# Performance work log

Hardware: AMD Instinct MI355X
Metric: run time of the kernel (lower is better)

Reference implementation:

```python
import jax, jax.numpy as jnp
import numpy as np

N, D, K = 8192, 4096, 8
F_HID = D // 4  # 1024


def setup_inputs() -> dict:
    key = jax.random.key(0)
    ks = jax.random.split(key, 8)
    s1 = 1.0 / np.sqrt(2 * D)
    s2 = 1.0 / np.sqrt(F_HID)
    sr = 1.0 / np.sqrt(D)
    return {
        "h_anchor": jax.random.normal(ks[0], (N, D), jnp.float32),
        "h_mask": jax.random.normal(ks[1], (N, D), jnp.float32),
        "Wr": jax.random.normal(ks[2], (K, D), jnp.float32) * sr,
        "br": jnp.zeros((K,), jnp.float32),
        "W1": jax.random.normal(ks[3], (K, F_HID, 2 * D), jnp.float32) * s1,
        "b1": jnp.zeros((K, F_HID), jnp.float32),
        "W2": jax.random.normal(ks[4], (K, D, F_HID), jnp.float32) * s2,
        "b2": jnp.zeros((K, D), jnp.float32),
    }


def reference(h_anchor, h_mask, Wr, br, W1, b1, W2, b2):
    # routing weights: softmax(h_mask @ Wr^T + br) -> [N, K]
    weights = jax.nn.softmax(h_mask @ Wr.T + br, axis=-1)
    # conditioned input: [N, 2D]
    conditioned = jnp.concatenate([h_anchor, h_mask], axis=-1)
    # all-expert first GEMM: [K, N, F]
    h1 = jnp.einsum("nc,kfc->knf", conditioned, W1) + b1[:, None, :]
    h1 = jax.nn.gelu(h1, approximate=False)  # torch nn.GELU default = exact erf
    # second GEMM: [K, N, D]
    expert_out = jnp.einsum("knf,kdf->knd", h1, W2) + b2[:, None, :]
    # softmax-weighted combine over experts -> [N, D]
    return jnp.einsum("knd,nk->nd", expert_out, weights)
```

## Files before the change

### kernel.cpp

```cpp
#include <hip/hip_runtime.h>
#include <hip/hip_bf16.h>
#include <math.h>

typedef __bf16 bf16_t;
typedef __bf16 bf16x4 __attribute__((ext_vector_type(4)));
typedef __bf16 bf16x8 __attribute__((ext_vector_type(8)));
typedef float  f32x4  __attribute__((ext_vector_type(4)));
typedef float  f32x16 __attribute__((ext_vector_type(16)));

#define AS1 __attribute__((address_space(1)))
#define AS3 __attribute__((address_space(3)))

__device__ __forceinline__ void gload_lds16(const bf16_t* g, char* l) {
  __builtin_amdgcn_global_load_lds((const AS1 void*)g, (AS3 void*)l, 16, 0, 0);
}

static constexpr int N_ROWS = 8192;
static constexpr int DDIM   = 4096;
static constexpr int KEXP   = 8;
static constexpr int FHID   = 1024;
static constexpr int KD     = 8192;
static constexpr int NKT    = KD / 64;


__global__ __launch_bounds__(256)
void routing_kernel(const float* __restrict__ hm, const float* __restrict__ Wr,
                    const float* __restrict__ br, float* __restrict__ wgt) {
  const int n = blockIdx.x;
  const int t = threadIdx.x;
  const int wid = t >> 6;
  const float4* row = (const float4*)(hm + (size_t)n * DDIM);
  float4 x[4];
#pragma unroll
  for (int j = 0; j < 4; ++j) x[j] = row[t + j * 256];
  __shared__ float red[KEXP][4];
  float part[KEXP];
#pragma unroll
  for (int k = 0; k < KEXP; ++k) {
    const float4* wr = (const float4*)(Wr + (size_t)k * DDIM);
    float s = 0.f;
#pragma unroll
    for (int j = 0; j < 4; ++j) {
      float4 w4 = wr[t + j * 256];
      s += x[j].x * w4.x + x[j].y * w4.y + x[j].z * w4.z + x[j].w * w4.w;
    }
#pragma unroll
    for (int off = 32; off > 0; off >>= 1) s += __shfl_down(s, off);
    part[k] = s;
  }
  if ((t & 63) == 0) {
#pragma unroll
    for (int k = 0; k < KEXP; ++k) red[k][wid] = part[k];
  }
  __syncthreads();
  if (t == 0) {
    float lg[KEXP];
    float mx = -1e30f;
#pragma unroll
    for (int k = 0; k < KEXP; ++k) {
      lg[k] = red[k][0] + red[k][1] + red[k][2] + red[k][3] + br[k];
      mx = fmaxf(mx, lg[k]);
    }
    float sum = 0.f;
#pragma unroll
    for (int k = 0; k < KEXP; ++k) { lg[k] = expf(lg[k] - mx); sum += lg[k]; }
    float inv = 1.f / sum;
#pragma unroll
    for (int k = 0; k < KEXP; ++k) wgt[(size_t)n * KEXP + k] = lg[k] * inv;
  }
}

__device__ __forceinline__ bf16x4 cvt4(float4 v) {
  bf16x4 o;
  o[0] = (bf16_t)v.x; o[1] = (bf16_t)v.y; o[2] = (bf16_t)v.z; o[3] = (bf16_t)v.w;
  return o;
}

__global__ __launch_bounds__(256)
void pack_cond_kernel(const float* __restrict__ ha, const float* __restrict__ hm,
                      bf16_t* __restrict__ Apk) {
  const int bm = blockIdx.x >> 7, t = blockIdx.x & 127;
  const int tid = threadIdx.x;
  const float* src = (t < 64) ? ha : hm;
  const int cb = (t & 63) * 64;
  __shared__ char pb[32768];
#pragma unroll
  for (int i = 0; i < 16; ++i) {
    int u = i * 256 + tid;
    int r = u >> 4, c = (u & 15) * 4;
    float4 v = *(const float4*)(src + (size_t)(bm * 256 + r) * DDIM + cb + c);
    int off = ((r >> 7) & 1) * 16384 + ((c >> 4) & 3) * 4096 + ((r >> 5) & 3) * 1024
            + ((c >> 3) & 1) * 512 + (r & 31) * 16 + (c & 7) * 2;
    *(bf16x4*)(pb + off) = cvt4(v);
  }
  __syncthreads();
  char* dst = (char*)Apk + (size_t)blockIdx.x * 32768;
#pragma unroll
  for (int i = 0; i < 8; ++i) {
    int off = i * 4096 + tid * 16;
    *(float4*)(dst + off) = *(const float4*)(pb + off);
  }
}

__global__ __launch_bounds__(256)
void pack_w1_kernel(const float* __restrict__ W1, bf16_t* __restrict__ Bpk) {
  const int bn = blockIdx.x >> 7, t = blockIdx.x & 127;
  const int tid = threadIdx.x;
  __shared__ char pb[32768];
#pragma unroll
  for (int i = 0; i < 16; ++i) {
    int u = i * 256 + tid;
    int r = u >> 4, c = (u & 15) * 4;
    float4 v = *(const float4*)(W1 + (size_t)(bn * 256 + r) * KD + t * 64 + c);
    int off = ((c >> 4) & 3) * 8192 + ((r >> 5) & 7) * 1024
            + ((c >> 3) & 1) * 512 + (r & 31) * 16 + (c & 7) * 2;
    *(bf16x4*)(pb + off) = cvt4(v);
  }
  __syncthreads();
  char* dst = (char*)Bpk + (size_t)blockIdx.x * 32768;
#pragma unroll
  for (int i = 0; i < 8; ++i) {
    int off = i * 4096 + tid * 16;
    *(float4*)(dst + off) = *(const float4*)(pb + off);
  }
}

__global__ __launch_bounds__(256)
void pack_w2_kernel(const float* __restrict__ W2, bf16_t* __restrict__ Bpk) {
  const int bn = blockIdx.x >> 7, t = blockIdx.x & 127;
  const int tid = threadIdx.x;
  const int ke = t >> 4, f0 = (t & 15) * 64;
  __shared__ char pb[32768];
#pragma unroll
  for (int i = 0; i < 16; ++i) {
    int u = i * 256 + tid;
    int r = u >> 4, c = (u & 15) * 4;
    float4 v = *(const float4*)(W2 + ((size_t)ke * DDIM + bn * 256 + r) * FHID + f0 + c);
    int off = ((c >> 4) & 3) * 8192 + ((r >> 5) & 7) * 1024
            + ((c >> 3) & 1) * 512 + (r & 31) * 16 + (c & 7) * 2;
    *(bf16x4*)(pb + off) = cvt4(v);
  }
  __syncthreads();
  char* dst = (char*)Bpk + (size_t)blockIdx.x * 32768;
#pragma unroll
  for (int i = 0; i < 8; ++i) {
    int off = i * 4096 + tid * 16;
    *(float4*)(dst + off) = *(const float4*)(pb + off);
  }
}

template <int MODE, int NCOLS>
__global__ __launch_bounds__(256, 1)
void gemm256_kernel(const bf16_t* __restrict__ Apk, const bf16_t* __restrict__ Bpk,
                    void* __restrict__ Cout, const float* __restrict__ bias,
                    const float* __restrict__ wgt) {
  __shared__ char lds_raw[2 * 65536];

  const int tid  = threadIdx.x;
  const int wid  = tid >> 6;
  const int lane = tid & 63;
  const int wr   = wid >> 1;
  const int wc   = wid & 1;

  constexpr int NBN    = NCOLS / 256;
  constexpr int NWIN_N = NBN / 16;
  const int bid = blockIdx.x;
  const int w   = bid >> 8;
  const int sl  = bid & 255;
  const int xcd = sl & 7;
  const int cu  = sl >> 3;
  const int wm  = w / NWIN_N, wn = w % NWIN_N;
  const int bm  = wm * 16 + ((xcd >> 1) << 2) + (cu & 3);
  const int bn  = wn * 16 + ((xcd & 1) << 3) + (cu >> 2);
  const int arow0 = bm * 256;
  const int brow0 = bn * 256;

  const size_t abase = (size_t)bm * NKT * 16384;
  const size_t bbase = (size_t)bn * NKT * 16384;
  const size_t ssub  = (size_t)(wid * 512 + lane * 8);
  const int    dsto  = wid << 10;

  const char* A0 = lds_raw + wr * 16384 + lane * 16;
  const char* B0 = lds_raw + 32768 + wc * 4096 + lane * 16;
  const char* A1 = A0 + 65536;
  const char* B1 = B0 + 65536;

  f32x16 acc[4][4];
#pragma unroll
  for (int mi = 0; mi < 4; ++mi)
#pragma unroll
    for (int nj = 0; nj < 4; ++nj)
#pragma unroll
      for (int r = 0; r < 16; ++r) acc[mi][nj][r] = 0.f;

  bf16x8 xa0, xa1, xa2, xa3, xb0, xb1, xb2, xb3;
  bf16x8 ya0, ya1, ya2, ya3, yb0, yb1, yb2, yb3;

#define SB __builtin_amdgcn_sched_barrier(0);
#define LG0 asm volatile("s_waitcnt lgkmcnt(0)" ::: "memory"); SB

#define STGA(C, TAU, NB)                                                         \
  gload_lds16(Apk + abase + (size_t)((TAU) & (NKT - 1)) * 16384 + (C) * 2048 + ssub, \
              (NB) + (C) * 4096 + dsto);
#define STGB(C, TAU, NB)                                                         \
  gload_lds16(Bpk + bbase + (size_t)((TAU) & (NKT - 1)) * 16384 + (C) * 2048 + ssub, \
              (NB) + 32768 + (C) * 4096 + dsto);

#define RDA4(P, BASE, S)                                                        \
  P##a0 = *(const bf16x8*)((BASE) + (S) * 4096);                                \
  P##a1 = *(const bf16x8*)((BASE) + (S) * 4096 + 1024);                         \
  P##a2 = *(const bf16x8*)((BASE) + (S) * 4096 + 2048);                         \
  P##a3 = *(const bf16x8*)((BASE) + (S) * 4096 + 3072);                         \
  SB
#define RDB4(P, BASE, S)                                                        \
  P##b0 = *(const bf16x8*)((BASE) + (S) * 8192);                                \
  P##b1 = *(const bf16x8*)((BASE) + (S) * 8192 + 1024);                         \
  P##b2 = *(const bf16x8*)((BASE) + (S) * 8192 + 2048);                         \
  P##b3 = *(const bf16x8*)((BASE) + (S) * 8192 + 3072);                         \
  SB

#define MF4(P, MI)                                                              \
  acc[MI][0] = __builtin_amdgcn_mfma_f32_32x32x16_bf16(P##a##MI, P##b0,         \
                                                       acc[MI][0], 0, 0, 0);    \
  acc[MI][1] = __builtin_amdgcn_mfma_f32_32x32x16_bf16(P##a##MI, P##b1,         \
                                                       acc[MI][1], 0, 0, 0);    \
  acc[MI][2] = __builtin_amdgcn_mfma_f32_32x32x16_bf16(P##a##MI, P##b2,         \
                                                       acc[MI][2], 0, 0, 0);    \
  acc[MI][3] = __builtin_amdgcn_mfma_f32_32x32x16_bf16(P##a##MI, P##b3,         \
                                                       acc[MI][3], 0, 0, 0);    \
  SB

#define TILE(T, CA, CB, NB)                                                     \
  RDA4(x, CA, 0) RDB4(x, CB, 0)                                                 \
  LG0                                                                           \
  MF4(x, 0) RDA4(y, CA, 1)                                                      \
  MF4(x, 1) RDB4(y, CB, 1)                                                      \
  MF4(x, 2) STGA(0, (T) + 1, NB) STGA(1, (T) + 1, NB)                           \
            STGA(2, (T) + 1, NB) STGA(3, (T) + 1, NB) SB                        \
  MF4(x, 3) STGA(4, (T) + 1, NB) STGA(5, (T) + 1, NB)                           \
            STGA(6, (T) + 1, NB) STGA(7, (T) + 1, NB) SB                        \
  LG0                                                                           \
  MF4(y, 0) RDA4(x, CA, 2)                                                      \
  MF4(y, 1) RDB4(x, CB, 2)                                                      \
  MF4(y, 2) STGB(0, (T) + 1, NB) STGB(1, (T) + 1, NB)                           \
            STGB(2, (T) + 1, NB) STGB(3, (T) + 1, NB) SB                        \
  MF4(y, 3) STGB(4, (T) + 1, NB) STGB(5, (T) + 1, NB)                           \
            STGB(6, (T) + 1, NB) STGB(7, (T) + 1, NB) SB                        \
  LG0                                                                           \
  MF4(x, 0) RDA4(y, CA, 3)                                                      \
  MF4(x, 1) RDB4(y, CB, 3)                                                      \
  MF4(x, 2) MF4(x, 3)                                                           \
  LG0                                                                           \
  MF4(y, 0) MF4(y, 1) MF4(y, 2) MF4(y, 3)                                       \
  asm volatile("s_waitcnt vmcnt(0)" ::: "memory");                              \
  SB                                                                            \
  __builtin_amdgcn_s_barrier();                                                 \
  SB

#pragma unroll
  for (int c = 0; c < 8; ++c) { STGA(c, 0, lds_raw) }
#pragma unroll
  for (int c = 0; c < 8; ++c) { STGB(c, 0, lds_raw) }
  asm volatile("s_waitcnt vmcnt(0)" ::: "memory");
  __builtin_amdgcn_s_barrier();
  SB

  for (int t = 0; t < NKT; t += 2) {
    TILE(t, A0, B0, lds_raw + 65536)
    TILE(t + 1, A1, B1, lds_raw)
  }
#undef TILE
#undef MF4
#undef RDA4
#undef RDB4
#undef STGA
#undef STGB
#undef LG0
#undef SB

  const int rbase = arow0 + wr * 128 + ((lane >> 5) << 2);
  const int cbase = brow0 + wc * 128 + (lane & 31);

  if constexpr (MODE == 1) {
    char* __restrict__ Hc = (char*)Cout;
    const int kexp = brow0 >> 10;
    float bv[4];
    size_t cpart[4];
#pragma unroll
    for (int nj = 0; nj < 4; ++nj) {
      int c = cbase + nj * 32;
      bv[nj] = bias[c];
      cpart[nj] = (size_t)(c >> 6) * 32768 + ((c >> 4) & 3) * 4096
                + ((c >> 3) & 1) * 512 + (c & 7) * 2;
    }
#pragma unroll
    for (int mi = 0; mi < 4; ++mi)
#pragma unroll
      for (int r = 0; r < 16; ++r) {
        int n = rbase + mi * 32 + (r & 3) + 8 * (r >> 2);
        float wn4 = wgt[(size_t)n * KEXP + kexp];
        size_t npart = (size_t)(n >> 8) * (NKT * 32768) + ((n >> 7) & 1) * 16384
                     + ((n >> 5) & 3) * 1024 + (n & 31) * 16;
#pragma unroll
        for (int nj = 0; nj < 4; ++nj) {
          float x = acc[mi][nj][r] + bv[nj];
          float g = 0.5f * x * (1.f + erff(x * 0.70710678118654752f));
          *(bf16_t*)(Hc + npart + cpart[nj]) = (bf16_t)(g * wn4);
        }
      }
  } else {
    float* __restrict__ O = (float*)Cout;
    float bc[4][KEXP];
#pragma unroll
    for (int nj = 0; nj < 4; ++nj)
#pragma unroll
      for (int k = 0; k < KEXP; ++k)
        bc[nj][k] = bias[(size_t)k * NCOLS + cbase + nj * 32];
#pragma unroll
    for (int mi = 0; mi < 4; ++mi)
#pragma unroll
      for (int r = 0; r < 16; ++r) {
        int n = rbase + mi * 32 + (r & 3) + 8 * (r >> 2);
        const float4* wp = (const float4*)(wgt + (size_t)n * KEXP);
        float4 wa = wp[0], wb = wp[1];
        float w8[KEXP] = {wa.x, wa.y, wa.z, wa.w, wb.x, wb.y, wb.z, wb.w};
#pragma unroll
        for (int nj = 0; nj < 4; ++nj) {
          float s = 0.f;
#pragma unroll
          for (int k = 0; k < KEXP; ++k) s += w8[k] * bc[nj][k];
          O[(size_t)n * NCOLS + cbase + nj * 32] = acc[mi][nj][r] + s;
        }
      }
  }
}

extern "C" void kernel_launch(void* const* d_in, const int* in_sizes, int n_in,
                              void* d_out, int out_size, void* d_ws, size_t ws_size,
                              hipStream_t stream) {
  const float* h_anchor = (const float*)d_in[0];
  const float* h_mask   = (const float*)d_in[1];
  const float* Wr       = (const float*)d_in[2];
  const float* br       = (const float*)d_in[3];
  const float* W1       = (const float*)d_in[4];
  const float* b1       = (const float*)d_in[5];
  const float* W2       = (const float*)d_in[6];
  const float* b2       = (const float*)d_in[7];
  float* out = (float*)d_out;

  char* ws = (char*)d_ws;
  bf16_t* Apk  = (bf16_t*)(ws);
  bf16_t* B1pk = (bf16_t*)(ws + ((size_t)128 << 20));
  bf16_t* B2pk = (bf16_t*)(ws + ((size_t)256 << 20));
  bf16_t* Hpk  = (bf16_t*)(ws + ((size_t)320 << 20));
  float*  wgt  = (float*) (ws + ((size_t)448 << 20));

  routing_kernel<<<N_ROWS, 256, 0, stream>>>(h_mask, Wr, br, wgt);
  pack_cond_kernel<<<32 * 128, 256, 0, stream>>>(h_anchor, h_mask, Apk);
  pack_w1_kernel<<<32 * 128, 256, 0, stream>>>(W1, B1pk);
  pack_w2_kernel<<<16 * 128, 256, 0, stream>>>(W2, B2pk);

  gemm256_kernel<1, 8192><<<(N_ROWS / 256) * (KD / 256), 256, 0, stream>>>(
      Apk, B1pk, (void*)Hpk, b1, wgt);
  gemm256_kernel<2, 4096><<<(N_ROWS / 256) * (DDIM / 256), 256, 0, stream>>>(
      Hpk, B2pk, (void*)out, b2, wgt);
}
```

Baseline: 1.789 ms.

## Restructure GEMM to 256x128 tiles with 512 threads and triple-buffered K=32 pipeline

```diff
diff --git a/kernel.cpp b/kernel.cpp
--- a/kernel.cpp
+++ b/kernel.cpp
@@ -6,7 +6,6 @@
 typedef __bf16 bf16x4 __attribute__((ext_vector_type(4)));
 typedef __bf16 bf16x8 __attribute__((ext_vector_type(8)));
 typedef float  f32x4  __attribute__((ext_vector_type(4)));
-typedef float  f32x16 __attribute__((ext_vector_type(16)));
 
 #define AS1 __attribute__((address_space(1)))
 #define AS3 __attribute__((address_space(3)))
@@ -20,7 +19,8 @@
 static constexpr int KEXP   = 8;
 static constexpr int FHID   = 1024;
 static constexpr int KD     = 8192;
-static constexpr int NKT    = KD / 64;
+static constexpr int NKT64  = KD / 64;
+static constexpr int NKT32  = KD / 32;
 
 
 __global__ __launch_bounds__(256)
@@ -150,11 +150,11 @@
 }
 
 template <int MODE, int NCOLS>
-__global__ __launch_bounds__(256, 1)
-void gemm256_kernel(const bf16_t* __restrict__ Apk, const bf16_t* __restrict__ Bpk,
-                    void* __restrict__ Cout, const float* __restrict__ bias,
-                    const float* __restrict__ wgt) {
-  __shared__ char lds_raw[2 * 65536];
+__global__ __launch_bounds__(512, 4)
+void gemm_kernel(const bf16_t* __restrict__ Apk, const bf16_t* __restrict__ Bpk,
+                 void* __restrict__ Cout, const float* __restrict__ bias,
+                 const float* __restrict__ wgt) {
+  __shared__ char lds[3 * 24576];
 
   const int tid  = threadIdx.x;
   const int wid  = tid >> 6;
@@ -162,7 +162,7 @@
   const int wr   = wid >> 1;
   const int wc   = wid & 1;
 
-  constexpr int NBN    = NCOLS / 256;
+  constexpr int NBN    = NCOLS / 128;
   constexpr int NWIN_N = NBN / 16;
   const int bid = blockIdx.x;
   const int w   = bid >> 8;
@@ -173,122 +173,116 @@
   const int bm  = wm * 16 + ((xcd >> 1) << 2) + (cu & 3);
   const int bn  = wn * 16 + ((xcd & 1) << 3) + (cu >> 2);
   const int arow0 = bm * 256;
-  const int brow0 = bn * 256;
-
-  const size_t abase = (size_t)bm * NKT * 16384;
-  const size_t bbase = (size_t)bn * NKT * 16384;
-  const size_t ssub  = (size_t)(wid * 512 + lane * 8);
-  const int    dsto  = wid << 10;
-
-  const char* A0 = lds_raw + wr * 16384 + lane * 16;
-  const char* B0 = lds_raw + 32768 + wc * 4096 + lane * 16;
-  const char* A1 = A0 + 65536;
-  const char* B1 = B0 + 65536;
-
-  f32x16 acc[4][4];
+  const int bcol0 = bn * 128;
+
+  const char* Abase = (const char*)Apk + (size_t)bm * NKT64 * 32768;
+  const char* Bbase = (const char*)Bpk + (size_t)(bn >> 1) * NKT64 * 32768;
+  const int pA0 = 2 * wid, pA1 = 2 * wid + 1, qB = wid;
+  const int a0s = (pA0 >> 3) * 16384 + ((pA0 >> 2) & 1) * 4096 + (pA0 & 3) * 1024;
+  const int a1s = (pA1 >> 3) * 16384 + ((pA1 >> 2) & 1) * 4096 + (pA1 & 3) * 1024;
+  const int a0d = (pA0 >> 3) * 8192 + ((pA0 >> 2) & 1) * 4096 + (pA0 & 3) * 1024;
+  const int a1d = (pA1 >> 3) * 8192 + ((pA1 >> 2) & 1) * 4096 + (pA1 & 3) * 1024;
+  const int bqs = (qB >> 2) * 8192 + ((bn & 1) * 4 + (qB & 3)) * 1024;
+  const int bqd = 16384 + (qB >> 2) * 4096 + (qB & 3) * 1024;
+
+  const int lpart = (lane & 15) * 16 + ((lane >> 4) & 1) * 512 + (lane >> 5) * 4096;
+  int aoff[4], boff[4];
 #pragma unroll
   for (int mi = 0; mi < 4; ++mi)
-#pragma unroll
-    for (int nj = 0; nj < 4; ++nj)
-#pragma unroll
-      for (int r = 0; r < 16; ++r) acc[mi][nj][r] = 0.f;
-
-  bf16x8 xa0, xa1, xa2, xa3, xb0, xb1, xb2, xb3;
-  bf16x8 ya0, ya1, ya2, ya3, yb0, yb1, yb2, yb3;
+    aoff[mi] = (wr >> 1) * 8192 + ((wr & 1) * 2 + (mi >> 1)) * 1024 + (mi & 1) * 256 + lpart;
+#pragma unroll
+  for (int nj = 0; nj < 4; ++nj)
+    boff[nj] = 16384 + (wc * 2 + (nj >> 1)) * 1024 + (nj & 1) * 256 + lpart;
+
+  f32x4 acc[4][4];
+  f32x4 zero = {0.f, 0.f, 0.f, 0.f};
+#pragma unroll
+  for (int mi = 0; mi < 4; ++mi)
+#pragma unroll
+    for (int nj = 0; nj < 4; ++nj) acc[mi][nj] = zero;
 
 #define SB __builtin_amdgcn_sched_barrier(0);
-#define LG0 asm volatile("s_waitcnt lgkmcnt(0)" ::: "memory"); SB
-
-#define STGA(C, TAU, NB)                                                         \
-  gload_lds16(Apk + abase + (size_t)((TAU) & (NKT - 1)) * 16384 + (C) * 2048 + ssub, \
-              (NB) + (C) * 4096 + dsto);
-#define STGB(C, TAU, NB)                                                         \
-  gload_lds16(Bpk + bbase + (size_t)((TAU) & (NKT - 1)) * 16384 + (C) * 2048 + ssub, \
-              (NB) + 32768 + (C) * 4096 + dsto);
-
-#define RDA4(P, BASE, S)                                                        \
-  P##a0 = *(const bf16x8*)((BASE) + (S) * 4096);                                \
-  P##a1 = *(const bf16x8*)((BASE) + (S) * 4096 + 1024);                         \
-  P##a2 = *(const bf16x8*)((BASE) + (S) * 4096 + 2048);                         \
-  P##a3 = *(const bf16x8*)((BASE) + (S) * 4096 + 3072);                         \
+#define STG3(KT, BUF)                                                            \
+  {                                                                              \
+    const int kt_ = (KT) & (NKT32 - 1);                                          \
+    const size_t t64 = (size_t)(kt_ >> 1) * 32768;                               \
+    const int klo = (kt_ & 1) * 2;                                               \
+    gload_lds16((const bf16_t*)(Abase + t64 + a0s + klo * 4096 + lane * 16),     \
+                (BUF) + a0d);                                                    \
+    gload_lds16((const bf16_t*)(Abase + t64 + a1s + klo * 4096 + lane * 16),     \
+                (BUF) + a1d);                                                    \
+    gload_lds16((const bf16_t*)(Bbase + t64 + bqs + klo * 8192 + lane * 16),     \
+                (BUF) + bqd);                                                    \
+  }
+
+  STG3(0, lds) STG3(1, lds + 24576) SB
+  asm volatile("s_waitcnt vmcnt(3)" ::: "memory");
   SB
-#define RDB4(P, BASE, S)                                                        \
-  P##b0 = *(const bf16x8*)((BASE) + (S) * 8192);                                \
-  P##b1 = *(const bf16x8*)((BASE) + (S) * 8192 + 1024);                         \
-  P##b2 = *(const bf16x8*)((BASE) + (S) * 8192 + 2048);                         \
-  P##b3 = *(const bf16x8*)((BASE) + (S) * 8192 + 3072);                         \
-  SB
-
-#define MF4(P, MI)                                                              \
-  acc[MI][0] = __builtin_amdgcn_mfma_f32_32x32x16_bf16(P##a##MI, P##b0,         \
-                                                       acc[MI][0], 0, 0, 0);    \
-  acc[MI][1] = __builtin_amdgcn_mfma_f32_32x32x16_bf16(P##a##MI, P##b1,         \
-                                                       acc[MI][1], 0, 0, 0);    \
-  acc[MI][2] = __builtin_amdgcn_mfma_f32_32x32x16_bf16(P##a##MI, P##b2,         \
-                                                       acc[MI][2], 0, 0, 0);    \
-  acc[MI][3] = __builtin_amdgcn_mfma_f32_32x32x16_bf16(P##a##MI, P##b3,         \
-                                                       acc[MI][3], 0, 0, 0);    \
-  SB
-
-#define TILE(T, CA, CB, NB)                                                     \
-  RDA4(x, CA, 0) RDB4(x, CB, 0)                                                 \
-  LG0                                                                           \
-  MF4(x, 0) RDA4(y, CA, 1)                                                      \
-  MF4(x, 1) RDB4(y, CB, 1)                                                      \
-  MF4(x, 2) STGA(0, (T) + 1, NB) STGA(1, (T) + 1, NB)                           \
-            STGA(2, (T) + 1, NB) STGA(3, (T) + 1, NB) SB                        \
-  MF4(x, 3) STGA(4, (T) + 1, NB) STGA(5, (T) + 1, NB)                           \
-            STGA(6, (T) + 1, NB) STGA(7, (T) + 1, NB) SB                        \
-  LG0                                                                           \
-  MF4(y, 0) RDA4(x, CA, 2)                                                      \
-  MF4(y, 1) RDB4(x, CB, 2)                                                      \
-  MF4(y, 2) STGB(0, (T) + 1, NB) STGB(1, (T) + 1, NB)                           \
-            STGB(2, (T) + 1, NB) STGB(3, (T) + 1, NB) SB                        \
-  MF4(y, 3) STGB(4, (T) + 1, NB) STGB(5, (T) + 1, NB)                           \
-            STGB(6, (T) + 1, NB) STGB(7, (T) + 1, NB) SB                        \
-  LG0                                                                           \
-  MF4(x, 0) RDA4(y, CA, 3)                                                      \
-  MF4(x, 1) RDB4(y, CB, 3)                                                      \
-  MF4(x, 2) MF4(x, 3)                                                           \
-  LG0                                                                           \
-  MF4(y, 0) MF4(y, 1) MF4(y, 2) MF4(y, 3)                                       \
-  asm volatile("s_waitcnt vmcnt(0)" ::: "memory");                              \
-  SB                                                                            \
-  __builtin_amdgcn_s_barrier();                                                 \
-  SB
-
-#pragma unroll
-  for (int c = 0; c < 8; ++c) { STGA(c, 0, lds_raw) }
-#pragma unroll
-  for (int c = 0; c < 8; ++c) { STGB(c, 0, lds_raw) }
-  asm volatile("s_waitcnt vmcnt(0)" ::: "memory");
   __builtin_amdgcn_s_barrier();
   SB
 
-  for (int t = 0; t < NKT; t += 2) {
-    TILE(t, A0, B0, lds_raw + 65536)
-    TILE(t + 1, A1, B1, lds_raw)
-  }
-#undef TILE
-#undef MF4
-#undef RDA4
-#undef RDB4
-#undef STGA
-#undef STGB
-#undef LG0
+  char* rb = lds;
+  char* mb = lds + 24576;
+  char* sb = lds + 49152;
+
+#pragma unroll 1
+  for (int t = 0; t < NKT32; ++t) {
+    STG3(t + 2, sb) SB
+    bf16x8 a0, a1, a2, a3, b0, b1, b2, b3;
+    a0 = *(const bf16x8*)(rb + aoff[0]); SB
+    a1 = *(const bf16x8*)(rb + aoff[1]); SB
+    a2 = *(const bf16x8*)(rb + aoff[2]); SB
+    a3 = *(const bf16x8*)(rb + aoff[3]); SB
+    b0 = *(const bf16x8*)(rb + boff[0]); SB
+    b1 = *(const bf16x8*)(rb + boff[1]); SB
+    b2 = *(const bf16x8*)(rb + boff[2]); SB
+    b3 = *(const bf16x8*)(rb + boff[3]); SB
+    __builtin_amdgcn_s_setprio(1);
+    asm volatile("s_waitcnt lgkmcnt(3)" ::: "memory"); SB
+    acc[0][0] = __builtin_amdgcn_mfma_f32_16x16x32_bf16(a0, b0, acc[0][0], 0, 0, 0);
+    acc[1][0] = __builtin_amdgcn_mfma_f32_16x16x32_bf16(a1, b0, acc[1][0], 0, 0, 0);
+    acc[2][0] = __builtin_amdgcn_mfma_f32_16x16x32_bf16(a2, b0, acc[2][0], 0, 0, 0);
+    acc[3][0] = __builtin_amdgcn_mfma_f32_16x16x32_bf16(a3, b0, acc[3][0], 0, 0, 0);
+    SB
+    asm volatile("s_waitcnt lgkmcnt(2)" ::: "memory"); SB
+    acc[0][1] = __builtin_amdgcn_mfma_f32_16x16x32_bf16(a0, b1, acc[0][1], 0, 0, 0);
+    acc[1][1] = __builtin_amdgcn_mfma_f32_16x16x32_bf16(a1, b1, acc[1][1], 0, 0, 0);
+    acc[2][1] = __builtin_amdgcn_mfma_f32_16x16x32_bf16(a2, b1, acc[2][1], 0, 0, 0);
+    acc[3][1] = __builtin_amdgcn_mfma_f32_16x16x32_bf16(a3, b1, acc[3][1], 0, 0, 0);
+    SB
+    asm volatile("s_waitcnt lgkmcnt(1)" ::: "memory"); SB
+    acc[0][2] = __builtin_amdgcn_mfma_f32_16x16x32_bf16(a0, b2, acc[0][2], 0, 0, 0);
+    acc[1][2] = __builtin_amdgcn_mfma_f32_16x16x32_bf16(a1, b2, acc[1][2], 0, 0, 0);
+    acc[2][2] = __builtin_amdgcn_mfma_f32_16x16x32_bf16(a2, b2, acc[2][2], 0, 0, 0);
+    acc[3][2] = __builtin_amdgcn_mfma_f32_16x16x32_bf16(a3, b2, acc[3][2], 0, 0, 0);
+    SB
+    asm volatile("s_waitcnt lgkmcnt(0)" ::: "memory"); SB
+    acc[0][3] = __builtin_amdgcn_mfma_f32_16x16x32_bf16(a0, b3, acc[0][3], 0, 0, 0);
+    acc[1][3] = __builtin_amdgcn_mfma_f32_16x16x32_bf16(a1, b3, acc[1][3], 0, 0, 0);
+    acc[2][3] = __builtin_amdgcn_mfma_f32_16x16x32_bf16(a2, b3, acc[2][3], 0, 0, 0);
+    acc[3][3] = __builtin_amdgcn_mfma_f32_16x16x32_bf16(a3, b3, acc[3][3], 0, 0, 0);
+    SB
+    __builtin_amdgcn_s_setprio(0);
+    asm volatile("s_waitcnt vmcnt(3)" ::: "memory");
+    SB
+    __builtin_amdgcn_s_barrier();
+    SB
+    char* tmp = rb; rb = mb; mb = sb; sb = tmp;
+  }
+#undef STG3
 #undef SB
 
-  const int rbase = arow0 + wr * 128 + ((lane >> 5) << 2);
-  const int cbase = brow0 + wc * 128 + (lane & 31);
+  const int rbase = arow0 + wr * 64 + ((lane >> 4) << 2);
+  const int cbase = bcol0 + wc * 64 + (lane & 15);
 
   if constexpr (MODE == 1) {
     char* __restrict__ Hc = (char*)Cout;
-    const int kexp = brow0 >> 10;
+    const int kexp = bcol0 >> 10;
     float bv[4];
     size_t cpart[4];
 #pragma unroll
     for (int nj = 0; nj < 4; ++nj) {
-      int c = cbase + nj * 32;
+      int c = cbase + nj * 16;
       bv[nj] = bias[c];
       cpart[nj] = (size_t)(c >> 6) * 32768 + ((c >> 4) & 3) * 4096
                 + ((c >> 3) & 1) * 512 + (c & 7) * 2;
@@ -296,10 +290,10 @@
 #pragma unroll
     for (int mi = 0; mi < 4; ++mi)
 #pragma unroll
-      for (int r = 0; r < 16; ++r) {
-        int n = rbase + mi * 32 + (r & 3) + 8 * (r >> 2);
+      for (int r = 0; r < 4; ++r) {
+        int n = rbase + mi * 16 + r;
         float wn4 = wgt[(size_t)n * KEXP + kexp];
-        size_t npart = (size_t)(n >> 8) * (NKT * 32768) + ((n >> 7) & 1) * 16384
+        size_t npart = (size_t)(n >> 8) * (NKT64 * 32768) + ((n >> 7) & 1) * 16384
                      + ((n >> 5) & 3) * 1024 + (n & 31) * 16;
 #pragma unroll
         for (int nj = 0; nj < 4; ++nj) {
@@ -315,12 +309,12 @@
     for (int nj = 0; nj < 4; ++nj)
 #pragma unroll
       for (int k = 0; k < KEXP; ++k)
-        bc[nj][k] = bias[(size_t)k * NCOLS + cbase + nj * 32];
+        bc[nj][k] = bias[(size_t)k * NCOLS + cbase + nj * 16];
 #pragma unroll
     for (int mi = 0; mi < 4; ++mi)
 #pragma unroll
-      for (int r = 0; r < 16; ++r) {
-        int n = rbase + mi * 32 + (r & 3) + 8 * (r >> 2);
+      for (int r = 0; r < 4; ++r) {
+        int n = rbase + mi * 16 + r;
         const float4* wp = (const float4*)(wgt + (size_t)n * KEXP);
         float4 wa = wp[0], wb = wp[1];
         float w8[KEXP] = {wa.x, wa.y, wa.z, wa.w, wb.x, wb.y, wb.z, wb.w};
@@ -329,7 +323,7 @@
           float s = 0.f;
 #pragma unroll
           for (int k = 0; k < KEXP; ++k) s += w8[k] * bc[nj][k];
-          O[(size_t)n * NCOLS + cbase + nj * 32] = acc[mi][nj][r] + s;
+          O[(size_t)n * NCOLS + cbase + nj * 16] = acc[mi][nj][r] + s;
         }
       }
   }
@@ -360,8 +354,8 @@
   pack_w1_kernel<<<32 * 128, 256, 0, stream>>>(W1, B1pk);
   pack_w2_kernel<<<16 * 128, 256, 0, stream>>>(W2, B2pk);
 
-  gemm256_kernel<1, 8192><<<(N_ROWS / 256) * (KD / 256), 256, 0, stream>>>(
+  gemm_kernel<1, 8192><<<(N_ROWS / 256) * (KD / 128), 512, 0, stream>>>(
       Apk, B1pk, (void*)Hpk, b1, wgt);
-  gemm256_kernel<2, 4096><<<(N_ROWS / 256) * (DDIM / 256), 256, 0, stream>>>(
+  gemm_kernel<2, 4096><<<(N_ROWS / 256) * (DDIM / 128), 512, 0, stream>>>(
       Hpk, B2pk, (void*)out, b2, wgt);
 }
```

New measurement: 1.611 ms. 10.0% less time.
